# Optimization experiments

Measured on AMD Instinct MI355X. Metric: run time of the kernel, lower is better.

The kernel has to match this reference:

```python
import jax, jax.numpy as jnp
import numpy as np

EMBED_DIM = 2048
NUM_HEADS = 16
HEAD_DIM = EMBED_DIM // NUM_HEADS
B, T = 4, 2048


def setup_inputs() -> dict:
    key = jax.random.key(0)
    ks = jax.random.split(key, 9)
    s = 1.0 / np.sqrt(EMBED_DIM)
    x = jax.random.normal(ks[0], (B, T, EMBED_DIM), dtype=jnp.float32)
    Wq = jax.random.normal(ks[1], (EMBED_DIM, EMBED_DIM), dtype=jnp.float32) * s
    bq = jnp.zeros((EMBED_DIM,), dtype=jnp.float32)
    Wk = jax.random.normal(ks[2], (EMBED_DIM, EMBED_DIM), dtype=jnp.float32) * s
    bk = jnp.zeros((EMBED_DIM,), dtype=jnp.float32)
    Wv = jax.random.normal(ks[3], (EMBED_DIM, EMBED_DIM), dtype=jnp.float32) * s
    bv = jnp.zeros((EMBED_DIM,), dtype=jnp.float32)
    Wo = jax.random.normal(ks[4], (EMBED_DIM, EMBED_DIM), dtype=jnp.float32) * s
    bo = jnp.zeros((EMBED_DIM,), dtype=jnp.float32)
    return {"x": x, "Wq": Wq, "bq": bq, "Wk": Wk, "bk": bk,
            "Wv": Wv, "bv": bv, "Wo": Wo, "bo": bo}


def reference(x, Wq, bq, Wk, bk, Wv, bv, Wo, bo):
    Bb, Tt, C = x.shape
    H, D = NUM_HEADS, C // NUM_HEADS
    # QKV projections (Linear: x @ W.T + b), reshape to [B, H, T, D]
    q = (jnp.einsum('btc,oc->bto', x, Wq) + bq).reshape(Bb, Tt, H, D).transpose(0, 2, 1, 3)
    k = (jnp.einsum('btc,oc->bto', x, Wk) + bk).reshape(Bb, Tt, H, D).transpose(0, 2, 1, 3)
    v = (jnp.einsum('btc,oc->bto', x, Wv) + bv).reshape(Bb, Tt, H, D).transpose(0, 2, 1, 3)
    logits = jnp.einsum('bhqd,bhkd->bhqk', q, k) / jnp.sqrt(jnp.float32(D))
    causal = jnp.triu(jnp.ones((Tt, Tt), dtype=bool), 1)  # True above diagonal
    logits = jnp.where(causal, -jnp.inf, logits)
    attn = jax.nn.softmax(logits, axis=-1)
    out = jnp.einsum('bhqk,bhkd->bhqd', attn, v)  # [B, H, T, D]
    out = out.transpose(0, 2, 1, 3).reshape(Bb, Tt, C)
    y = jnp.einsum('btc,oc->bto', out, Wo) + bo
    return y
```

## Files before the change

kernel.cpp:

```cpp
#include <hip/hip_runtime.h>
#include <hip/hip_bf16.h>
#include <cstdint>
#include <cstddef>

typedef __attribute__((ext_vector_type(8))) short short8;
typedef __attribute__((ext_vector_type(4))) short short4_;
typedef __attribute__((ext_vector_type(4))) float floatx4;
typedef __attribute__((ext_vector_type(4))) unsigned short ushort4_;

#define MFMA16(a, b, c) __builtin_amdgcn_mfma_f32_16x16x32_bf16((a), (b), (c), 0, 0, 0)

__device__ __forceinline__ unsigned short f2bf(float f) {
  __hip_bfloat16 h = __float2bfloat16(f);
  return *reinterpret_cast<unsigned short*>(&h);
}

__device__ __forceinline__ float exp2_fast(float x) {
  float r;
  asm("v_exp_f32 %0, %1" : "=v"(r) : "v"(x));
  return r;
}

__device__ __forceinline__ void gl_lds16(const void* g, void* lds) {
  __builtin_amdgcn_global_load_lds(
      (const __attribute__((address_space(1))) void*)g,
      (__attribute__((address_space(3))) void*)lds, 16, 0, 0);
}

__global__ void cast5_f32_bf16(const float* __restrict__ x, const float* __restrict__ wq,
                               const float* __restrict__ wk, const float* __restrict__ wv,
                               const float* __restrict__ wo,
                               __hip_bfloat16* __restrict__ xb, __hip_bfloat16* __restrict__ wqb,
                               __hip_bfloat16* __restrict__ wkb, __hip_bfloat16* __restrict__ wvb,
                               __hip_bfloat16* __restrict__ wob) {
  const int bid = blockIdx.x;
  const float* src;
  __hip_bfloat16* dst;
  int base;
  if (bid < 16384)      { src = x;  dst = xb;  base = bid; }
  else if (bid < 20480) { src = wq; dst = wqb; base = bid - 16384; }
  else if (bid < 24576) { src = wk; dst = wkb; base = bid - 20480; }
  else if (bid < 28672) { src = wv; dst = wvb; base = bid - 24576; }
  else                  { src = wo; dst = wob; base = bid - 28672; }
  const int i = base * 1024 + threadIdx.x * 4;
  const float4 v = *reinterpret_cast<const float4*>(src + i);
  ushort4_ o = { f2bf(v.x), f2bf(v.y), f2bf(v.z), f2bf(v.w) };
  *reinterpret_cast<ushort4_*>(dst + i) = o;
}

template <int MODE>
__global__ __launch_bounds__(512, 2)
void gemm256p(const __hip_bfloat16* __restrict__ Ap, const __hip_bfloat16* __restrict__ Bp,
              const float* __restrict__ bias, void* __restrict__ Cout,
              int M, int N, int K) {
  __shared__ __align__(16) __hip_bfloat16 SA[4][256 * 32];
  __shared__ __align__(16) __hip_bfloat16 SB[4][256 * 32];

  const int tid = threadIdx.x;
  const int wid = tid >> 6, lane = tid & 63;
  const int wr = wid >> 2, wc = wid & 3;
  const int g = lane >> 4, c16 = lane & 15;

  const int nbn = N >> 8;
  const int cpx = gridDim.x >> 3;
  const int swzb = (blockIdx.x & 7) * cpx + (blockIdx.x >> 3);
  const int bm = swzb / nbn, bn = swzb % nbn;

  const int srow = lane >> 2;
  const int slog = (lane & 3) ^ ((lane >> 3) & 3);
  const int swz = c16 * 32 + (g ^ ((c16 >> 1) & 3)) * 8;

  floatx4 acc[8][4] = {};
  short8 afA[4], afB[4], bf[4];

  auto stage_i = [&](int kt, int i) {
    const int kb = kt * 32;
    const int slot = kt & 3;
    const int rbase = i * 128 + wid * 16;
    gl_lds16(Ap + (size_t)(bm * 256 + rbase + srow) * K + kb + slog * 8,
             SA[slot] + rbase * 32);
    gl_lds16(Bp + (size_t)(bn * 256 + rbase + srow) * K + kb + slog * 8,
             SB[slot] + rbase * 32);
  };

  auto readA = [&](int slot, int half, short8* af) {
    const __hip_bfloat16* sa = SA[slot];
#pragma unroll
    for (int m = 0; m < 4; ++m)
      af[m] = *reinterpret_cast<const short8*>(sa + wr * 4096 + (half * 4 + m) * 512 + swz);
  };
  auto readB = [&](int slot) {
    const __hip_bfloat16* sb = SB[slot];
#pragma unroll
    for (int n = 0; n < 4; ++n)
      bf[n] = *reinterpret_cast<const short8*>(sb + wc * 2048 + n * 512 + swz);
  };
  auto mfma16 = [&](short8* af, int mh) {
    __builtin_amdgcn_s_setprio(1);
#pragma unroll
    for (int m = 0; m < 4; ++m)
#pragma unroll
      for (int n = 0; n < 4; ++n)
        acc[mh * 4 + m][n] = MFMA16(af[m], bf[n], acc[mh * 4 + m][n]);
    __builtin_amdgcn_s_setprio(0);
  };

  const int nkt = K >> 5;
  stage_i(0, 0); stage_i(0, 1);
  stage_i(1, 0); stage_i(1, 1);
  stage_i(2, 0); stage_i(2, 1);
  asm volatile("s_waitcnt vmcnt(8)" ::: "memory");
  __builtin_amdgcn_s_barrier();

  for (int kt = 0; kt < nkt - 3; ++kt) {
    const int s = kt & 3;
    readA(s, 0, afA);
    readB(s);
    stage_i(kt + 3, 0);
    asm volatile("" ::: "memory");
    __builtin_amdgcn_s_barrier();
    mfma16(afA, 0);
    asm volatile("" ::: "memory");
    __builtin_amdgcn_s_barrier();
    readA(s, 1, afB);
    stage_i(kt + 3, 1);
    asm volatile("s_waitcnt vmcnt(8)" ::: "memory");
    __builtin_amdgcn_s_barrier();
    mfma16(afB, 1);
    asm volatile("" ::: "memory");
    __builtin_amdgcn_s_barrier();
  }
#pragma unroll
  for (int t = 0; t < 3; ++t) {
    const int kt = nkt - 3 + t;
    const int s = kt & 3;
    readA(s, 0, afA);
    readB(s);
    asm volatile("" ::: "memory");
    __builtin_amdgcn_s_barrier();
    mfma16(afA, 0);
    asm volatile("" ::: "memory");
    __builtin_amdgcn_s_barrier();
    readA(s, 1, afB);
    if (t == 0) asm volatile("s_waitcnt vmcnt(4)" ::: "memory");
    else if (t == 1) asm volatile("s_waitcnt vmcnt(0)" ::: "memory");
    __builtin_amdgcn_s_barrier();
    mfma16(afB, 1);
    asm volatile("" ::: "memory");
    __builtin_amdgcn_s_barrier();
  }

#pragma unroll
  for (int n = 0; n < 4; ++n) {
    const int colg = bn * 256 + wc * 64 + n * 16 + c16;
    const float bv = bias[colg];
#pragma unroll
    for (int m = 0; m < 8; ++m) {
      const int rowg = bm * 256 + wr * 128 + m * 16 + g * 4;
      if (MODE == 0) {
        __hip_bfloat16* C = (__hip_bfloat16*)Cout;
#pragma unroll
        for (int j = 0; j < 4; ++j)
          C[(size_t)(rowg + j) * N + colg] = __float2bfloat16(acc[m][n][j] + bv);
      } else if (MODE == 1) {
        __hip_bfloat16* C = (__hip_bfloat16*)Cout;
        const int bb = rowg >> 11, t0 = rowg & 2047;
        ushort4_ pk = { f2bf(acc[m][n][0] + bv), f2bf(acc[m][n][1] + bv),
                        f2bf(acc[m][n][2] + bv), f2bf(acc[m][n][3] + bv) };
        *reinterpret_cast<ushort4_*>(C + ((size_t)bb * 2048 + colg) * 2048 + t0) = pk;
      } else {
        float* C = (float*)Cout;
#pragma unroll
        for (int j = 0; j < 4; ++j)
          C[(size_t)(rowg + j) * N + colg] = acc[m][n][j] + bv;
      }
    }
  }
}

__global__ __launch_bounds__(256, 2)
void attn_fwd12(const __hip_bfloat16* __restrict__ Q, const __hip_bfloat16* __restrict__ K,
                const __hip_bfloat16* __restrict__ Vt, __hip_bfloat16* __restrict__ ctx) {
  constexpr int T = 2048, C = 2048, D = 128;
  __shared__ __align__(16) __hip_bfloat16 Ks[64 * 128];
  __shared__ __align__(16) __hip_bfloat16 Vs[128 * 64];
  __shared__ __align__(16) __hip_bfloat16 Pl[4][16 * 64];

  const int tid = threadIdx.x;
  const int w = tid >> 6, lane = tid & 63;
  const int g = lane >> 4, c16 = lane & 15;

  const int bid = blockIdx.x;
  const int x = bid & 7;
  const int i = bid >> 3;
  const int lo = i & 3, hi = i >> 5;
  const int bh = x * 8 + ((i >> 2) & 7);
  const int qb = (int)((0xF12C4A97865B3DE0ull >> (4 * (hi * 4 + lo))) & 15);
  const int b = bh >> 4, h = bh & 15;
  const int wq = qb * 128 + w * 32;

  const __hip_bfloat16* Qh = Q + (size_t)b * T * C + h * D;
  const __hip_bfloat16* Kh = K + (size_t)b * T * C + h * D;
  const __hip_bfloat16* Vh = Vt + (size_t)bh * D * T;

  const float scale2 = 0.12751744f;

  short8 qf[2][4];
#pragma unroll
  for (int m = 0; m < 2; ++m)
#pragma unroll
    for (int kk = 0; kk < 4; ++kk) {
      short8 v = *reinterpret_cast<const short8*>(Qh + (size_t)(wq + m * 16 + c16) * C + kk * 32 + g * 8);
      short8 r;
#pragma unroll
      for (int e = 0; e < 8; ++e) {
        unsigned short u = (unsigned short)v[e];
        __hip_bfloat16 bh16 = *reinterpret_cast<__hip_bfloat16*>(&u);
        r[e] = (short)f2bf(__bfloat162float(bh16) * scale2);
      }
      qf[m][kk] = r;
    }

  floatx4 acc[2][8] = {};
  float mrow[2] = {-INFINITY, -INFINITY};
  float lrow[2] = {0.f, 0.f};

  const int krow = tid >> 4;
  const int kslot = (tid & 15) ^ (krow & 7);
  const int kgcol = (tid & 15) * 8;
  const int vrow = tid >> 3;
  const int vslot = (tid & 7) ^ (vrow & 7);
  const int vgcol = (tid & 7) * 8;

  short8 kr[4], vr[4];
  auto gloadK = [&](int kb) {
#pragma unroll
    for (int p = 0; p < 4; ++p)
      kr[p] = *reinterpret_cast<const short8*>(Kh + (size_t)(kb + p * 16 + krow) * C + kgcol);
  };
  auto gloadV = [&](int kb) {
#pragma unroll
    for (int p = 0; p < 4; ++p)
      vr[p] = *reinterpret_cast<const short8*>(Vh + (size_t)(p * 32 + vrow) * T + kb + vgcol);
  };

  __hip_bfloat16* Pq = Pl[w];
  const int nkt = qb * 2 + 2;
  gloadK(0);
  gloadV(0);

  for (int kt = 0; kt < nkt; ++kt) {
    const int kb = kt * 64;
    __syncthreads();
#pragma unroll
    for (int p = 0; p < 4; ++p)
      *reinterpret_cast<short8*>(&Ks[(p * 16 + krow) * 128 + kslot * 8]) = kr[p];
#pragma unroll
    for (int p = 0; p < 4; ++p)
      *reinterpret_cast<short8*>(&Vs[(p * 32 + vrow) * 64 + vslot * 8]) = vr[p];
    __syncthreads();

    const bool hasnext = (kt + 1 < nkt);
    const bool part = (kb <= wq + 31);
    if (hasnext) gloadK(kb + 64);

    short8 pb[2][2];
    if (part) {
      floatx4 s[2][4] = {};
      __builtin_amdgcn_s_setprio(1);
#pragma unroll
      for (int n = 0; n < 4; ++n)
#pragma unroll
        for (int kk = 0; kk < 4; ++kk) {
          short8 kf = *reinterpret_cast<const short8*>(
              &Ks[(n * 16 + c16) * 128 + (((kk * 4 + g) ^ (c16 & 7)) * 8)]);
          s[0][n] = MFMA16(kf, qf[0][kk], s[0][n]);
          s[1][n] = MFMA16(kf, qf[1][kk], s[1][n]);
        }
      __builtin_amdgcn_s_setprio(0);

      const bool needmask = (kb + 63 > wq);
      float vmax[2];
      if (needmask) {
#pragma unroll
        for (int m = 0; m < 2; ++m) {
          const int q = wq + m * 16 + c16;
          float vm = -INFINITY;
#pragma unroll
          for (int n = 0; n < 4; ++n)
#pragma unroll
            for (int j = 0; j < 4; ++j) {
              float a = s[m][n][j];
              if (kb + n * 16 + g * 4 + j > q) a = -INFINITY;
              s[m][n][j] = a;
              vm = fmaxf(vm, a);
            }
          vmax[m] = vm;
        }
      } else {
#pragma unroll
        for (int m = 0; m < 2; ++m) {
          float v0 = fmaxf(fmaxf(s[m][0][0], s[m][0][1]), fmaxf(s[m][0][2], s[m][0][3]));
          float v1 = fmaxf(fmaxf(s[m][1][0], s[m][1][1]), fmaxf(s[m][1][2], s[m][1][3]));
          float v2 = fmaxf(fmaxf(s[m][2][0], s[m][2][1]), fmaxf(s[m][2][2], s[m][2][3]));
          float v3 = fmaxf(fmaxf(s[m][3][0], s[m][3][1]), fmaxf(s[m][3][2], s[m][3][3]));
          vmax[m] = fmaxf(fmaxf(v0, v1), fmaxf(v2, v3));
        }
      }
#pragma unroll
      for (int m = 0; m < 2; ++m) {
        vmax[m] = fmaxf(vmax[m], __shfl_xor(vmax[m], 16));
        vmax[m] = fmaxf(vmax[m], __shfl_xor(vmax[m], 32));
      }
      const float grow = fmaxf(vmax[0] - mrow[0], vmax[1] - mrow[1]);
      const bool nore = __all(grow <= 8.0f);
#pragma unroll
      for (int m = 0; m < 2; ++m) {
        const float mn = nore ? mrow[m] : fmaxf(mrow[m], vmax[m]);
        float rs = 0.f;
#pragma unroll
        for (int n = 0; n < 4; ++n) {
          float p0 = exp2_fast(s[m][n][0] - mn), p1 = exp2_fast(s[m][n][1] - mn);
          float p2 = exp2_fast(s[m][n][2] - mn), p3 = exp2_fast(s[m][n][3] - mn);
          rs += (p0 + p1) + (p2 + p3);
          ushort4_ pk = { f2bf(p0), f2bf(p1), f2bf(p2), f2bf(p3) };
          *reinterpret_cast<ushort4_*>(&Pq[c16 * 64 + (((4 * n + g) ^ c16) * 4)]) = pk;
        }
        rs += __shfl_xor(rs, 16);
        rs += __shfl_xor(rs, 32);
        if (nore) {
          lrow[m] += rs;
        } else {
          const float sc = exp2_fast(mrow[m] - mn);
          lrow[m] = lrow[m] * sc + rs;
          mrow[m] = mn;
#pragma unroll
          for (int dt = 0; dt < 8; ++dt)
#pragma unroll
            for (int j = 0; j < 4; ++j) acc[m][dt][j] *= sc;
        }
#pragma unroll
        for (int ks = 0; ks < 2; ++ks) {
          short4_ lo2 = *reinterpret_cast<const short4_*>(&Pq[c16 * 64 + (((8 * ks + 2 * g) ^ c16) * 4)]);
          short4_ hi2 = *reinterpret_cast<const short4_*>(&Pq[c16 * 64 + (((8 * ks + 2 * g + 1) ^ c16) * 4)]);
          short8 r;
          r[0] = lo2[0]; r[1] = lo2[1]; r[2] = lo2[2]; r[3] = lo2[3];
          r[4] = hi2[0]; r[5] = hi2[1]; r[6] = hi2[2]; r[7] = hi2[3];
          pb[m][ks] = r;
        }
      }
    }
    if (hasnext) gloadV(kb + 64);
    if (part) {
      __builtin_amdgcn_s_setprio(1);
#pragma unroll
      for (int dt = 0; dt < 8; ++dt)
#pragma unroll
        for (int ks = 0; ks < 2; ++ks) {
          const int pslot = ((ks * 4 + g) ^ (c16 & 7)) * 8;
          short8 vf = *reinterpret_cast<const short8*>(&Vs[(dt * 16 + c16) * 64 + pslot]);
          acc[0][dt] = MFMA16(vf, pb[0][ks], acc[0][dt]);
          acc[1][dt] = MFMA16(vf, pb[1][ks], acc[1][dt]);
        }
      __builtin_amdgcn_s_setprio(0);
    }
  }

#pragma unroll
  for (int m = 0; m < 2; ++m) {
    const float inv = 1.0f / lrow[m];
    const size_t row = (size_t)b * T + wq + m * 16 + c16;
#pragma unroll
    for (int dt = 0; dt < 8; ++dt) {
      ushort4_ o = { f2bf(acc[m][dt][0] * inv), f2bf(acc[m][dt][1] * inv),
                     f2bf(acc[m][dt][2] * inv), f2bf(acc[m][dt][3] * inv) };
      *reinterpret_cast<ushort4_*>(ctx + row * C + h * D + dt * 16 + g * 4) = o;
    }
  }
}

extern "C" void kernel_launch(void* const* d_in, const int* in_sizes, int n_in,
                              void* d_out, int out_size, void* d_ws, size_t ws_size,
                              hipStream_t stream) {
  const float* x  = (const float*)d_in[0];
  const float* Wq = (const float*)d_in[1];
  const float* bq = (const float*)d_in[2];
  const float* Wk = (const float*)d_in[3];
  const float* bk = (const float*)d_in[4];
  const float* Wv = (const float*)d_in[5];
  const float* bv = (const float*)d_in[6];
  const float* Wo = (const float*)d_in[7];
  const float* bo = (const float*)d_in[8];

  const int M = 8192, N = 2048, K = 2048;
  const size_t MB = 1u << 20;
  char* ws = (char*)d_ws;
  __hip_bfloat16* xb  = (__hip_bfloat16*)(ws);
  __hip_bfloat16* wqb = (__hip_bfloat16*)(ws + 32 * MB);
  __hip_bfloat16* wkb = (__hip_bfloat16*)(ws + 40 * MB);
  __hip_bfloat16* wvb = (__hip_bfloat16*)(ws + 48 * MB);
  __hip_bfloat16* wob = (__hip_bfloat16*)(ws + 56 * MB);
  __hip_bfloat16* Qb  = (__hip_bfloat16*)(ws + 64 * MB);
  __hip_bfloat16* Kb  = (__hip_bfloat16*)(ws + 96 * MB);
  __hip_bfloat16* Vtb = (__hip_bfloat16*)(ws + 128 * MB);
  if (ws_size < 160 * MB) return;

  cast5_f32_bf16<<<32768, 256, 0, stream>>>(x, Wq, Wk, Wv, Wo, xb, wqb, wkb, wvb, wob);

  const dim3 gg((M / 256) * (N / 256));
  gemm256p<0><<<gg, 512, 0, stream>>>(xb, wqb, bq, Qb, M, N, K);
  gemm256p<0><<<gg, 512, 0, stream>>>(xb, wkb, bk, Kb, M, N, K);
  gemm256p<1><<<gg, 512, 0, stream>>>(xb, wvb, bv, Vtb, M, N, K);

  attn_fwd12<<<64 * 16, 256, 0, stream>>>(Qb, Kb, Vtb, xb);

  gemm256p<2><<<gg, 512, 0, stream>>>(xb, wob, bo, d_out, M, N, K);
}
```

Before: 446.7 us.

## Switch GEMM to K=64 tiles with double-buffered LDS and XOR swizzle

Restructures the projection GEMM's main loop. It now stages 64-wide K tiles into two LDS buffers instead of 32-wide tiles into a four-slot ring. The LDS swizzle changes to an 8-chunk XOR pattern, and each K tile runs four MFMA quarter-phases, interleaving the loads for the next tile. This halves the number of outer iterations and barriers per K element. The cost is a shallower prefetch distance (one tile ahead, with a full vmcnt(0) wait every iteration), so global load latency may be exposed more.

Result: no change. 440.4 us, median of 2 (-1.4%).

```diff
diff --git a/kernel.cpp b/kernel.cpp
--- a/kernel.cpp
+++ b/kernel.cpp
@@ -50,11 +50,11 @@
 
 template <int MODE>
 __global__ __launch_bounds__(512, 2)
-void gemm256p(const __hip_bfloat16* __restrict__ Ap, const __hip_bfloat16* __restrict__ Bp,
+void gemm256q(const __hip_bfloat16* __restrict__ Ap, const __hip_bfloat16* __restrict__ Bp,
               const float* __restrict__ bias, void* __restrict__ Cout,
               int M, int N, int K) {
-  __shared__ __align__(16) __hip_bfloat16 SA[4][256 * 32];
-  __shared__ __align__(16) __hip_bfloat16 SB[4][256 * 32];
+  __shared__ __align__(16) __hip_bfloat16 SA[2][256 * 64];
+  __shared__ __align__(16) __hip_bfloat16 SB[2][256 * 64];
 
   const int tid = threadIdx.x;
   const int wid = tid >> 6, lane = tid & 63;
@@ -66,87 +66,78 @@
   const int swzb = (blockIdx.x & 7) * cpx + (blockIdx.x >> 3);
   const int bm = swzb / nbn, bn = swzb % nbn;
 
-  const int srow = lane >> 2;
-  const int slog = (lane & 3) ^ ((lane >> 3) & 3);
-  const int swz = c16 * 32 + (g ^ ((c16 >> 1) & 3)) * 8;
+  const int srow8 = lane >> 3;
+  const int sc8 = lane & 7;
+  const int sgcol = (sc8 ^ srow8) * 8;
 
   floatx4 acc[8][4] = {};
-  short8 afA[4], afB[4], bf[4];
-
-  auto stage_i = [&](int kt, int i) {
-    const int kb = kt * 32;
-    const int slot = kt & 3;
-    const int rbase = i * 128 + wid * 16;
-    gl_lds16(Ap + (size_t)(bm * 256 + rbase + srow) * K + kb + slog * 8,
-             SA[slot] + rbase * 32);
-    gl_lds16(Bp + (size_t)(bn * 256 + rbase + srow) * K + kb + slog * 8,
-             SB[slot] + rbase * 32);
-  };
-
-  auto readA = [&](int slot, int half, short8* af) {
+  short8 af[4], bf[4];
+
+  auto stageA = [&](int p, int kt, int slot) {
+    const int ck = p * 8 + wid;
+    const int row = ck * 8 + srow8;
+    gl_lds16(Ap + (size_t)(bm * 256 + row) * K + kt * 64 + sgcol, SA[slot] + ck * 512);
+  };
+  auto stageB = [&](int p, int kt, int slot) {
+    const int ck = p * 8 + wid;
+    const int row = ck * 8 + srow8;
+    gl_lds16(Bp + (size_t)(bn * 256 + row) * K + kt * 64 + sgcol, SB[slot] + ck * 512);
+  };
+  auto readA = [&](int slot, int mh, int kk) {
     const __hip_bfloat16* sa = SA[slot];
 #pragma unroll
-    for (int m = 0; m < 4; ++m)
-      af[m] = *reinterpret_cast<const short8*>(sa + wr * 4096 + (half * 4 + m) * 512 + swz);
-  };
-  auto readB = [&](int slot) {
+    for (int mi = 0; mi < 4; ++mi)
+      af[mi] = *reinterpret_cast<const short8*>(
+          sa + (wr * 128 + (mh * 4 + mi) * 16 + c16) * 64 + (((kk * 4 + g) ^ (c16 & 7)) * 8));
+  };
+  auto readB = [&](int slot, int kk) {
     const __hip_bfloat16* sb = SB[slot];
 #pragma unroll
     for (int n = 0; n < 4; ++n)
-      bf[n] = *reinterpret_cast<const short8*>(sb + wc * 2048 + n * 512 + swz);
-  };
-  auto mfma16 = [&](short8* af, int mh) {
+      bf[n] = *reinterpret_cast<const short8*>(
+          sb + (wc * 64 + n * 16 + c16) * 64 + (((kk * 4 + g) ^ (c16 & 7)) * 8));
+  };
+  auto mfma_q = [&](int mh) {
     __builtin_amdgcn_s_setprio(1);
 #pragma unroll
-    for (int m = 0; m < 4; ++m)
+    for (int mi = 0; mi < 4; ++mi)
 #pragma unroll
       for (int n = 0; n < 4; ++n)
-        acc[mh * 4 + m][n] = MFMA16(af[m], bf[n], acc[mh * 4 + m][n]);
+        acc[mh * 4 + mi][n] = MFMA16(af[mi], bf[n], acc[mh * 4 + mi][n]);
     __builtin_amdgcn_s_setprio(0);
   };
 
-  const int nkt = K >> 5;
-  stage_i(0, 0); stage_i(0, 1);
-  stage_i(1, 0); stage_i(1, 1);
-  stage_i(2, 0); stage_i(2, 1);
-  asm volatile("s_waitcnt vmcnt(8)" ::: "memory");
+  const int nkt = K >> 6;
+#pragma unroll
+  for (int p = 0; p < 4; ++p) { stageA(p, 0, 0); stageB(p, 0, 0); }
+  asm volatile("s_waitcnt vmcnt(0)" ::: "memory");
   __builtin_amdgcn_s_barrier();
 
-  for (int kt = 0; kt < nkt - 3; ++kt) {
-    const int s = kt & 3;
-    readA(s, 0, afA);
-    readB(s);
-    stage_i(kt + 3, 0);
-    asm volatile("" ::: "memory");
-    __builtin_amdgcn_s_barrier();
-    mfma16(afA, 0);
-    asm volatile("" ::: "memory");
-    __builtin_amdgcn_s_barrier();
-    readA(s, 1, afB);
-    stage_i(kt + 3, 1);
-    asm volatile("s_waitcnt vmcnt(8)" ::: "memory");
-    __builtin_amdgcn_s_barrier();
-    mfma16(afB, 1);
-    asm volatile("" ::: "memory");
-    __builtin_amdgcn_s_barrier();
-  }
-#pragma unroll
-  for (int t = 0; t < 3; ++t) {
-    const int kt = nkt - 3 + t;
-    const int s = kt & 3;
-    readA(s, 0, afA);
-    readB(s);
-    asm volatile("" ::: "memory");
-    __builtin_amdgcn_s_barrier();
-    mfma16(afA, 0);
-    asm volatile("" ::: "memory");
-    __builtin_amdgcn_s_barrier();
-    readA(s, 1, afB);
-    if (t == 0) asm volatile("s_waitcnt vmcnt(4)" ::: "memory");
-    else if (t == 1) asm volatile("s_waitcnt vmcnt(0)" ::: "memory");
-    __builtin_amdgcn_s_barrier();
-    mfma16(afB, 1);
-    asm volatile("" ::: "memory");
+  for (int kt = 0; kt < nkt; ++kt) {
+    const int s = kt & 1;
+    const bool hn = (kt + 1 < nkt);
+    readA(s, 0, 0);
+    readB(s, 0);
+    if (hn) { stageA(0, kt + 1, s ^ 1); stageB(0, kt + 1, s ^ 1);
+              stageA(1, kt + 1, s ^ 1); stageB(1, kt + 1, s ^ 1); }
+    __builtin_amdgcn_s_barrier();
+    mfma_q(0);
+    __builtin_amdgcn_s_barrier();
+    readA(s, 1, 0);
+    if (hn) { stageA(2, kt + 1, s ^ 1); stageB(2, kt + 1, s ^ 1);
+              stageA(3, kt + 1, s ^ 1); stageB(3, kt + 1, s ^ 1); }
+    __builtin_amdgcn_s_barrier();
+    mfma_q(1);
+    __builtin_amdgcn_s_barrier();
+    readA(s, 0, 1);
+    readB(s, 1);
+    __builtin_amdgcn_s_barrier();
+    mfma_q(0);
+    __builtin_amdgcn_s_barrier();
+    readA(s, 1, 1);
+    __builtin_amdgcn_s_barrier();
+    mfma_q(1);
+    if (hn) asm volatile("s_waitcnt vmcnt(0)" ::: "memory");
     __builtin_amdgcn_s_barrier();
   }
 
@@ -408,11 +399,11 @@
   cast5_f32_bf16<<<32768, 256, 0, stream>>>(x, Wq, Wk, Wv, Wo, xb, wqb, wkb, wvb, wob);
 
   const dim3 gg((M / 256) * (N / 256));
-  gemm256p<0><<<gg, 512, 0, stream>>>(xb, wqb, bq, Qb, M, N, K);
-  gemm256p<0><<<gg, 512, 0, stream>>>(xb, wkb, bk, Kb, M, N, K);
-  gemm256p<1><<<gg, 512, 0, stream>>>(xb, wvb, bv, Vtb, M, N, K);
+  gemm256q<0><<<gg, 512, 0, stream>>>(xb, wqb, bq, Qb, M, N, K);
+  gemm256q<0><<<gg, 512, 0, stream>>>(xb, wkb, bk, Kb, M, N, K);
+  gemm256q<1><<<gg, 512, 0, stream>>>(xb, wvb, bv, Vtb, M, N, K);
 
   attn_fwd12<<<64 * 16, 256, 0, stream>>>(Qb, Kb, Vtb, xb);
 
-  gemm256p<2><<<gg, 512, 0, stream>>>(xb, wob, bo, d_out, M, N, K);
-}
+  gemm256q<2><<<gg, 512, 0, stream>>>(xb, wob, bo, d_out, M, N, K);
+}
```
